# Performance work log

Measured on AMD Instinct MI355X. Metric: run time of the kernel, lower is better.

The kernel has to match this reference:

```python
import jax, jax.numpy as jnp
import numpy as np

B, T, N, D, M, H, L, FF = 8, 128, 24, 128, 9, 8, 4, 1024
F = D // H          # spatial head dim = 16
HD = D // H         # temporal head dim = 16
ND = N * D          # 3072
NM = N * M          # 216


def setup_inputs() -> dict:
    key = jax.random.key(0)
    ks = jax.random.split(key, 24)
    w = lambda k, shape, s=0.05: (jax.random.normal(k, shape, jnp.float32) * s)
    z = lambda shape: jnp.zeros(shape, jnp.float32)
    return {
        "inputs": jax.random.normal(ks[0], (B, T, NM), jnp.float32),
        "emb_W": w(ks[1], (N, M, D)), "emb_b": z((N, D)),
        "sp_Wq": w(ks[2], (L, H, N, D, F)), "sp_bq": z((L, H, N, F)),
        "sp_Wk": w(ks[3], (L, H, D, F)), "sp_bk": z((L, H, F)),
        "sp_Wv": w(ks[4], (L, H, D, F)), "sp_bv": z((L, H, F)),
        "tmp_Win": w(ks[5], (L, N, 3 * D, D)), "tmp_bin": z((L, N, 3 * D)),
        "tmp_Wout": w(ks[6], (L, N, D, D)), "tmp_bout": z((L, N, D)),
        "ff_W1": w(ks[7], (L, ND, FF)), "ff_b1": z((L, FF)),
        "ff_W2": w(ks[8], (L, FF, ND)), "ff_b2": z((L, ND)),
        "ln_g": jnp.ones((L, ND), jnp.float32), "ln_b": z((L, ND)),
        "fin_W": w(ks[9], (ND, NM)), "fin_b": z((NM,)),
    }


def _ln(x, g, b):
    m = jnp.mean(x, -1, keepdims=True)
    v = jnp.mean(jnp.square(x - m), -1, keepdims=True)
    return (x - m) * jax.lax.rsqrt(v + 1e-5) * g + b


def _pos_encoding():
    # standard sinusoidal PE; original adds it over the FIRST axis of the
    # (B, T, N*D) tensor (applied before the permute), so index by B.
    pos = jnp.arange(B, dtype=jnp.float32)[:, None]
    div = jnp.exp(jnp.arange(0, ND, 2, dtype=jnp.float32) * (-np.log(10000.0) / ND))
    pe = jnp.zeros((B, ND), jnp.float32)
    pe = pe.at[:, 0::2].set(jnp.sin(pos * div)).at[:, 1::2].set(jnp.cos(pos * div))
    return pe


def reference(inputs, emb_W, emb_b, sp_Wq, sp_bq, sp_Wk, sp_bk, sp_Wv, sp_bv,
              tmp_Win, tmp_bin, tmp_Wout, tmp_bout, ff_W1, ff_b1, ff_W2, ff_b2,
              ln_g, ln_b, fin_W, fin_b):
    # joint embedding: (B,T,N,M) @ (N,M,D) -> (B,T,N,D)
    x4 = inputs.reshape(B, T, N, M)
    emb = (jnp.einsum('btnm,nmd->btnd', x4, emb_W) + emb_b).reshape(B, T, ND)
    emb = emb + _pos_encoding()[:, None, :]
    h = emb.transpose(1, 0, 2)                     # (T, B, ND)
    # PyTorch float attn_mask is ADDED to scores: +1.0 strictly below diagonal
    mask = jnp.tril(jnp.ones((T, T), jnp.float32), -1)
    for l in range(L):
        xr = h.reshape(T, B, N, D)
        # ---- spatial attention (shared K/V, per-joint Q, per head) ----
        k = jnp.einsum('tbnd,hdf->tbhnf', xr, sp_Wk[l]) + sp_bk[l][:, None, :]
        v = jnp.einsum('tbnd,hdf->tbhnf', xr, sp_Wv[l]) + sp_bv[l][:, None, :]
        q = jnp.einsum('tbnd,hndf->tbhnf', xr, sp_Wq[l]) + sp_bq[l]
        a = jax.nn.softmax(jnp.einsum('tbhnf,tbhmf->tbhnm', q, k) / jnp.sqrt(jnp.float32(F)), -1)
        sp = jnp.einsum('tbhnm,tbhmf->tbhnf', a, v)
        sp = sp.transpose(0, 1, 3, 2, 4).reshape(T, B, ND)   # joint-major, heads concat within joint
        sp = _ln(sp + h, ln_g[l], ln_b[l])
        # ---- temporal attention (per-joint nn.MultiheadAttention) ----
        Wq_t, Wk_t, Wv_t = tmp_Win[l, :, :D], tmp_Win[l, :, D:2 * D], tmp_Win[l, :, 2 * D:]
        bq_t, bk_t, bv_t = tmp_bin[l, :, :D], tmp_bin[l, :, D:2 * D], tmp_bin[l, :, 2 * D:]
        qt = (jnp.einsum('tbnd,ned->tbne', xr, Wq_t) + bq_t).reshape(T, B, N, H, HD)
        kt = (jnp.einsum('tbnd,ned->tbne', xr, Wk_t) + bk_t).reshape(T, B, N, H, HD)
        vt = (jnp.einsum('tbnd,ned->tbne', xr, Wv_t) + bv_t).reshape(T, B, N, H, HD)
        st = jnp.einsum('tbnhe,sbnhe->bnhts', qt, kt) / jnp.sqrt(jnp.float32(HD)) + mask
        at = jax.nn.softmax(st, -1)
        ot = jnp.einsum('bnhts,sbnhe->tbnhe', at, vt).reshape(T, B, N, D)
        tp = (jnp.einsum('tbnd,nod->tbno', ot, tmp_Wout[l]) + tmp_bout[l]).reshape(T, B, ND)
        tp = _ln(tp + h, ln_g[l], ln_b[l])
        # ---- FFN (no activation in original) + residual + shared LN ----
        a2 = sp + tp
        o = (a2 @ ff_W1[l] + ff_b1[l]) @ ff_W2[l] + ff_b2[l]
        h = _ln(o + a2, ln_g[l], ln_b[l])
    out = h @ fin_W + fin_b                        # (T, B, NM)
    return out.transpose(1, 0, 2) + inputs
```

## Files before the change

### kernel.cpp

```cpp
#include <hip/hip_runtime.h>
#include <hip/hip_bf16.h>
#include <math.h>

constexpr int kB = 8, kT = 128, kN = 24, kD = 128, kM = 9, kH = 8, kL = 4, kFF = 1024;
constexpr int kF = 16;
constexpr int kHD = 16;
constexpr int kND = kN * kD;
constexpr int kNM = kN * kM;
constexpr int kP = kB * kT;

using bf16x8 = __attribute__((ext_vector_type(8))) short;
using f32x4  = __attribute__((ext_vector_type(4))) float;
typedef __hip_bfloat16 bf16;

__device__ __forceinline__ void load_lds16(const void* g, void* l) {
  __builtin_amdgcn_global_load_lds(
      (const __attribute__((address_space(1))) void*)g,
      (__attribute__((address_space(3))) void*)l, 16, 0, 0);
}

template<int BM, int BN, bool OUTBF>
__global__ __launch_bounds__(256) void mfma_gemm(
    const bf16* __restrict__ A, const bf16* __restrict__ Bm,
    const float* __restrict__ bias, void* __restrict__ Cv,
    int M, int Nc, int K, int ldB, int sAi, int sCi,
    long offAg, long offBg, long offCg, int sBg)
{
  constexpr int WM = BM / 2, WN = BN / 2;
  constexpr int MT = WM / 16, NT = WN / 16;
  constexpr int ASLOTS = BM * 8;
  constexpr int BSLOTS = BN * 8;
  constexpr int CSTR = BN + 4;
  __shared__ __align__(16) char smem[(BM + BN) * 64 * 2];
  bf16* As = (bf16*)smem;
  bf16* Bs = (bf16*)(smem + BM * 64 * 2);
  float* Cs = (float*)smem;

  int g = blockIdx.z;
  A  += offAg * g;
  Bm += offBg * g;
  long cbase = offCg * (long)g;
  int bOff = sBg * g;

  int m0 = blockIdx.y * BM, n0 = blockIdx.x * BN;
  int tid = threadIdx.x, lane = tid & 63, wave = tid >> 6;
  int wm = wave >> 1, wn = wave & 1;
  int fr = lane & 15, fq = lane >> 4;

  f32x4 acc[MT][NT] = {};

  for (int kk = 0; kk < K; kk += 64) {
#pragma unroll
    for (int s = tid; s < ASLOTS; s += 256) {
      int m = s >> 3, kq = (s & 7) ^ (m & 7);
      load_lds16(A + (size_t)(m0 + m) * sAi + (kk + kq * 8), &As[s * 8]);
    }
#pragma unroll
    for (int s = tid; s < BSLOTS; s += 256) {
      int n = s >> 3, kq = (s & 7) ^ (n & 7);
      int nr = n0 + n; if (nr > Nc - 1) nr = Nc - 1;
      load_lds16(Bm + (size_t)nr * ldB + (kk + kq * 8), &Bs[s * 8]);
    }
    __syncthreads();
#pragma unroll
    for (int ks = 0; ks < 2; ks++) {
      bf16x8 af[MT], bfr[NT];
#pragma unroll
      for (int i = 0; i < MT; i++) {
        int row = wm * WM + i * 16 + fr;
        af[i] = *(const bf16x8*)&As[row * 64 + (((ks * 4 + fq) ^ (row & 7)) * 8)];
      }
#pragma unroll
      for (int j = 0; j < NT; j++) {
        int row = wn * WN + j * 16 + fr;
        bfr[j] = *(const bf16x8*)&Bs[row * 64 + (((ks * 4 + fq) ^ (row & 7)) * 8)];
      }
#pragma unroll
      for (int i = 0; i < MT; i++)
#pragma unroll
        for (int j = 0; j < NT; j++)
          acc[i][j] = __builtin_amdgcn_mfma_f32_16x16x32_bf16(af[i], bfr[j], acc[i][j], 0, 0, 0);
    }
    __syncthreads();
  }

  constexpr int NCHUNK = BN / 16;
  int tcol = tid & (NCHUNK - 1);
  int trow = tid / NCHUNK;
  int colbase = n0 + tcol * 16;
  float vb[16];
  if (trow < 32) {
#pragma unroll
    for (int jj = 0; jj < 16; jj++)
      vb[jj] = bias ? bias[bOff + colbase + jj] : 0.f;
  }
#pragma unroll
  for (int i = 0; i < MT; i++) {
    __syncthreads();
#pragma unroll
    for (int j = 0; j < NT; j++)
#pragma unroll
      for (int r = 0; r < 4; r++)
        Cs[(wm * 16 + fq * 4 + r) * CSTR + wn * WN + j * 16 + fr] = acc[i][j][r];
    __syncthreads();
    if (trow < 32) {
      int row = m0 + (trow >> 4) * WM + i * 16 + (trow & 15);
      float vals[16];
#pragma unroll
      for (int jj = 0; jj < 4; jj++)
        *(float4*)&vals[jj * 4] = *(const float4*)&Cs[trow * CSTR + tcol * 16 + jj * 4];
#pragma unroll
      for (int jj = 0; jj < 16; jj++) vals[jj] += vb[jj];
      if (OUTBF) {
        bf16* cp = (bf16*)Cv + cbase + (size_t)row * sCi + colbase;
        union { bf16 h[8]; uint4 v; } pk;
#pragma unroll
        for (int half = 0; half < 2; half++) {
          if (colbase + half * 8 + 8 <= Nc) {
#pragma unroll
            for (int jj = 0; jj < 8; jj++) pk.h[jj] = __float2bfloat16(vals[half * 8 + jj]);
            *(uint4*)(cp + half * 8) = pk.v;
          }
        }
      } else {
        float* cp = (float*)Cv + cbase + (size_t)row * sCi + colbase;
#pragma unroll
        for (int jj = 0; jj < 4; jj++)
          if (colbase + jj * 4 + 4 <= Nc) *(float4*)(cp + jj * 4) = *(float4*)&vals[jj * 4];
      }
    }
  }
}

constexpr int NB_EMB = kP;
constexpr int NB_SPQ = kL * kH * kN;
constexpr int NB_SPK = kL * kH * kN;
constexpr int NB_SPV = kL * kH * kN;
constexpr int NB_TMP = (kL * kN * 384 * kD / 8) / 256;
constexpr int NB_CVT = (kL * 24 * 128 * 128 / 8) / 256;
constexpr int NB_SPB = (kL * 24 * 768) / 256;
constexpr int NB_W1  = (kFF / 64) * (kND / 64) * kL;
constexpr int NB_W2  = (kND / 64) * (kFF / 64) * kL;
constexpr int NB_FIN = ((kNM + 63) / 64) * (kND / 64);
constexpr int OFF_SPQ = NB_EMB;
constexpr int OFF_SPK = OFF_SPQ + NB_SPQ;
constexpr int OFF_SPV = OFF_SPK + NB_SPK;
constexpr int OFF_TMP = OFF_SPV + NB_SPV;
constexpr int OFF_CVT = OFF_TMP + NB_TMP;
constexpr int OFF_SPB = OFF_CVT + NB_CVT;
constexpr int OFF_W1  = OFF_SPB + NB_SPB;
constexpr int OFF_W2  = OFF_W1 + NB_W1;
constexpr int OFF_FIN = OFF_W2 + NB_W2;
constexpr int NB_PREP = OFF_FIN + NB_FIN;

__device__ __forceinline__ void trans_cvt_body(
    const float* __restrict__ in, bf16* __restrict__ out,
    int R, int C, int bx, int by, float (*t)[65], int tid)
{
  int c0 = bx * 64, r0 = by * 64;
  for (int s = tid; s < 1024; s += 256) {
    int rr = s >> 4, c4 = (s & 15) * 4;
    int r = r0 + rr, c = c0 + c4;
    float4 v;
    if (c + 4 <= C) v = *(const float4*)&in[(size_t)r * C + c];
    else {
      float tmp[4];
#pragma unroll
      for (int j = 0; j < 4; j++) tmp[j] = (c + j < C) ? in[(size_t)r * C + c + j] : 0.f;
      v = *(float4*)tmp;
    }
    *(float4*)&t[rr][c4] = v;
  }
  __syncthreads();
  for (int s = tid; s < 512; s += 256) {
    int cc = s >> 3, r8 = (s & 7) * 8;
    int c = c0 + cc;
    if (c < C) {
      union { bf16 h[8]; uint4 v; } pk;
#pragma unroll
      for (int j = 0; j < 8; j++) pk.h[j] = __float2bfloat16(t[r8 + j][cc]);
      *(uint4*)&out[(size_t)c * R + r0 + r8] = pk.v;
    }
  }
}

__device__ __forceinline__ void spw_transpose_body(
    const float* __restrict__ src, bf16* __restrict__ dst, float* ts, int tid)
{
  for (int s = tid; s < 512; s += 256) {
    float4 v = ((const float4*)src)[s];
    int d = s >> 2, f4 = (s & 3) * 4;
    ts[(f4 + 0) * 132 + d] = v.x;
    ts[(f4 + 1) * 132 + d] = v.y;
    ts[(f4 + 2) * 132 + d] = v.z;
    ts[(f4 + 3) * 132 + d] = v.w;
  }
  __syncthreads();
  int f = tid >> 4, d8 = (tid & 15) * 8;
  float4 a = *(const float4*)&ts[f * 132 + d8];
  float4 b = *(const float4*)&ts[f * 132 + d8 + 4];
  union { bf16 h[8]; uint4 v; } pk;
  pk.h[0] = __float2bfloat16(a.x); pk.h[1] = __float2bfloat16(a.y);
  pk.h[2] = __float2bfloat16(a.z); pk.h[3] = __float2bfloat16(a.w);
  pk.h[4] = __float2bfloat16(b.x); pk.h[5] = __float2bfloat16(b.y);
  pk.h[6] = __float2bfloat16(b.z); pk.h[7] = __float2bfloat16(b.w);
  *(uint4*)&dst[(size_t)f * 128 + d8] = pk.v;
}

__global__ __launch_bounds__(256) void prep_kernel(
    const float* __restrict__ sp_Wq, const float* __restrict__ sp_Wk,
    const float* __restrict__ sp_Wv, const float* __restrict__ tmp_Win,
    bf16* __restrict__ spW,
    const float* __restrict__ tmp_Wout, bf16* __restrict__ toWb,
    const float* __restrict__ sp_bq, const float* __restrict__ sp_bk,
    const float* __restrict__ sp_bv, const float* __restrict__ tmp_bin,
    float* __restrict__ spbc,
    const float* __restrict__ ff_W1, bf16* __restrict__ W1t,
    const float* __restrict__ ff_W2, bf16* __restrict__ W2t,
    const float* __restrict__ fin_W, bf16* __restrict__ finWt,
    const float* __restrict__ inp, const float* __restrict__ emb_W,
    const float* __restrict__ emb_b, float* __restrict__ hb,
    bf16* __restrict__ hbb)
{
  __shared__ __align__(16) char sm[64 * 65 * 4];
  int bid = blockIdx.x, tid = threadIdx.x;

  if (bid < OFF_SPQ) {
    int p = bid;
    int t = p / kB, b = p % kB;
    float* xs = (float*)sm;
    if (tid < kNM)
      xs[tid] = inp[((size_t)b * kT + t) * kNM + tid];
    __syncthreads();
    const float c1 = -logf(10000.f) / (float)kND;
    for (int c4 = tid; c4 < kND / 4; c4 += 256) {
      int c = c4 * 4;
      int n = c >> 7, d = c & 127;
      float4 acc = *(const float4*)&emb_b[n * kD + d];
#pragma unroll
      for (int m = 0; m < kM; m++) {
        float xv = xs[n * kM + m];
        float4 w = *(const float4*)&emb_W[((size_t)(n * kM + m)) * kD + d];
        acc.x += xv * w.x; acc.y += xv * w.y; acc.z += xv * w.z; acc.w += xv * w.w;
      }
      float ang0 = (float)b * expf((float)c * c1);
      float ang1 = (float)b * expf((float)(c + 2) * c1);
      acc.x += sinf(ang0); acc.y += cosf(ang0);
      acc.z += sinf(ang1); acc.w += cosf(ang1);
      *(float4*)&hb[(size_t)p * kND + c] = acc;
      union { bf16 h4[4]; uint2 v; } pk;
      pk.h4[0] = __float2bfloat16(acc.x); pk.h4[1] = __float2bfloat16(acc.y);
      pk.h4[2] = __float2bfloat16(acc.z); pk.h4[3] = __float2bfloat16(acc.w);
      *(uint2*)&hbb[(size_t)p * kND + c] = pk.v;
    }
  } else if (bid < OFF_SPK) {
    int idx = bid - OFF_SPQ;
    int l = idx / 192, rem = idx % 192;
    int hh = rem / 24, n = rem % 24;
    const float* src = sp_Wq + ((((size_t)l * kH + hh) * kN + n)) * (kD * kF);
    bf16* dst = spW + (((size_t)(l * 24 + n)) * 768 + hh * 16) * 128;
    spw_transpose_body(src, dst, (float*)sm, tid);
  } else if (bid < OFF_SPV) {
    int idx = bid - OFF_SPK;
    int l = idx / 192, rem = idx % 192;
    int hh = rem / 24, n = rem % 24;
    const float* src = sp_Wk + (((size_t)l * kH + hh)) * (kD * kF);
    bf16* dst = spW + (((size_t)(l * 24 + n)) * 768 + 128 + hh * 16) * 128;
    spw_transpose_body(src, dst, (float*)sm, tid);
  } else if (bid < OFF_TMP) {
    int idx = bid - OFF_SPV;
    int l = idx / 192, rem = idx % 192;
    int hh = rem / 24, n = rem % 24;
    const float* src = sp_Wv + (((size_t)l * kH + hh)) * (kD * kF);
    bf16* dst = spW + (((size_t)(l * 24 + n)) * 768 + 256 + hh * 16) * 128;
    spw_transpose_body(src, dst, (float*)sm, tid);
  } else if (bid < OFF_CVT) {
    long j8 = ((long)(bid - OFF_TMP) * 256 + tid) * 8;
    long ln = j8 / 49152, rem = j8 % 49152;
    const float* src = &tmp_Win[ln * 49152 + rem];
    float4 v0 = *(const float4*)src, v1 = *(const float4*)(src + 4);
    union { bf16 h[8]; uint4 v; } pk;
    pk.h[0] = __float2bfloat16(v0.x); pk.h[1] = __float2bfloat16(v0.y);
    pk.h[2] = __float2bfloat16(v0.z); pk.h[3] = __float2bfloat16(v0.w);
    pk.h[4] = __float2bfloat16(v1.x); pk.h[5] = __float2bfloat16(v1.y);
    pk.h[6] = __float2bfloat16(v1.z); pk.h[7] = __float2bfloat16(v1.w);
    *(uint4*)&spW[ln * 98304 + 49152 + rem] = pk.v;
  } else if (bid < OFF_SPB) {
    int i8 = ((bid - OFF_CVT) * 256 + tid) * 8;
    float4 v0 = *(const float4*)(tmp_Wout + i8);
    float4 v1 = *(const float4*)(tmp_Wout + i8 + 4);
    union { bf16 h[8]; uint4 v; } pk;
    pk.h[0] = __float2bfloat16(v0.x); pk.h[1] = __float2bfloat16(v0.y);
    pk.h[2] = __float2bfloat16(v0.z); pk.h[3] = __float2bfloat16(v0.w);
    pk.h[4] = __float2bfloat16(v1.x); pk.h[5] = __float2bfloat16(v1.y);
    pk.h[6] = __float2bfloat16(v1.z); pk.h[7] = __float2bfloat16(v1.w);
    *(uint4*)(toWb + i8) = pk.v;
  } else if (bid < OFF_W1) {
    int i = (bid - OFF_SPB) * 256 + tid;
    int r = i % 768;
    int n = (i / 768) % 24;
    int l = i / (768 * 24);
    int hh = (r & 127) >> 4, f = r & 15;
    float v;
    if (r < 128)      v = sp_bq[(((size_t)l * kH + hh) * kN + n) * kF + f];
    else if (r < 256) v = sp_bk[((size_t)l * kH + hh) * kF + f];
    else if (r < 384) v = sp_bv[((size_t)l * kH + hh) * kF + f];
    else              v = tmp_bin[((size_t)l * kN + n) * 384 + (r - 384)];
    spbc[i] = v;
  } else if (bid < OFF_W2) {
    int id2 = bid - OFF_W1;
    int bz = id2 / (16 * 48);
    int rem = id2 % (16 * 48);
    trans_cvt_body(ff_W1 + (size_t)bz * kND * kFF, W1t + (size_t)bz * kFF * kND,
                   kND, kFF, rem % 16, rem / 16, (float(*)[65])sm, tid);
  } else if (bid < OFF_FIN) {
    int id2 = bid - OFF_W2;
    int bz = id2 / (48 * 16);
    int rem = id2 % (48 * 16);
    trans_cvt_body(ff_W2 + (size_t)bz * kFF * kND, W2t + (size_t)bz * kND * kFF,
                   kFF, kND, rem % 48, rem / 48, (float(*)[65])sm, tid);
  } else {
    int id2 = bid - OFF_FIN;
    trans_cvt_body(fin_W, finWt, kND, kNM, id2 % 4, id2 / 4, (float(*)[65])sm, tid);
  }
}

__global__ __launch_bounds__(256) void attn_kernel(
    const bf16* __restrict__ qkv, float* __restrict__ sp_out,
    bf16* __restrict__ ot)
{
  __shared__ __align__(16) char smem[39168];
  int tid = threadIdx.x;

  if (blockIdx.x < kP) {
    int p = blockIdx.x;
    float* s = (float*)smem;
    for (int i = tid; i < 2304; i += 256) {
      int n = i / 96, c4 = (i % 96) * 4;
      ushort4 u = *(const ushort4*)((const ushort*)qkv + ((size_t)n * kP + p) * 768 + c4);
      float4 f;
      f.x = __bfloat162float(*(const bf16*)&u.x);
      f.y = __bfloat162float(*(const bf16*)&u.y);
      f.z = __bfloat162float(*(const bf16*)&u.z);
      f.w = __bfloat162float(*(const bf16*)&u.w);
      *(float4*)&s[n * 388 + c4] = f;
    }
    __syncthreads();
    if (tid < 192) {
      int hh = tid / 24, n = tid % 24;
      const float4* qr = (const float4*)(s + n * 388 + hh * 16);
      float4 q0 = qr[0], q1 = qr[1], q2 = qr[2], q3 = qr[3];
      float sc[24];
      float mx = -1e30f;
#pragma unroll
      for (int m = 0; m < 24; m++) {
        const float4* kr = (const float4*)(s + m * 388 + 128 + hh * 16);
        float4 k0 = kr[0], k1 = kr[1], k2 = kr[2], k3 = kr[3];
        float d = q0.x * k0.x + q0.y * k0.y + q0.z * k0.z + q0.w * k0.w
                + q1.x * k1.x + q1.y * k1.y + q1.z * k1.z + q1.w * k1.w
                + q2.x * k2.x + q2.y * k2.y + q2.z * k2.z + q2.w * k2.w
                + q3.x * k3.x + q3.y * k3.y + q3.z * k3.z + q3.w * k3.w;
        d *= 0.25f;
        sc[m] = d;
        mx = fmaxf(mx, d);
      }
      float sum = 0.f;
#pragma unroll
      for (int m = 0; m < 24; m++) { float e = __expf(sc[m] - mx); sc[m] = e; sum += e; }
      float inv = 1.f / sum;
      float4 o0 = {0,0,0,0}, o1 = {0,0,0,0}, o2 = {0,0,0,0}, o3 = {0,0,0,0};
#pragma unroll
      for (int m = 0; m < 24; m++) {
        const float4* vr = (const float4*)(s + m * 388 + 256 + hh * 16);
        float4 v0 = vr[0], v1 = vr[1], v2 = vr[2], v3 = vr[3];
        float w = sc[m];
        o0.x += w * v0.x; o0.y += w * v0.y; o0.z += w * v0.z; o0.w += w * v0.w;
        o1.x += w * v1.x; o1.y += w * v1.y; o1.z += w * v1.z; o1.w += w * v1.w;
        o2.x += w * v2.x; o2.y += w * v2.y; o2.z += w * v2.z; o2.w += w * v2.w;
        o3.x += w * v3.x; o3.y += w * v3.y; o3.z += w * v3.z; o3.w += w * v3.w;
      }
      float* orow = sp_out + (size_t)p * kND + n * kD + hh * 16;
      o0.x *= inv; o0.y *= inv; o0.z *= inv; o0.w *= inv;
      o1.x *= inv; o1.y *= inv; o1.z *= inv; o1.w *= inv;
      o2.x *= inv; o2.y *= inv; o2.z *= inv; o2.w *= inv;
      o3.x *= inv; o3.y *= inv; o3.z *= inv; o3.w *= inv;
      *(float4*)(orow)      = o0;
      *(float4*)(orow + 4)  = o1;
      *(float4*)(orow + 8)  = o2;
      *(float4*)(orow + 12) = o3;
    }
  } else {
    int g = blockIdx.x - kP;
    int hh = g & 7, n = (g >> 3) % 24, b = g / 192;
    ushort (*Qs)[40]  = (ushort(*)[40])(smem);
    ushort (*Ks)[40]  = (ushort(*)[40])(smem + 10240);
    ushort (*Ps)[136] = (ushort(*)[136])(smem);
    ushort (*Vt)[136] = (ushort(*)[136])(smem + 34816);

    {
      int t = tid >> 1, e8 = (tid & 1) * 8;
      const ushort* src = (const ushort*)qkv +
          ((size_t)n * kP + (size_t)t * kB + b) * 768 + 384 + hh * 16 + e8;
      uint4 q = *(const uint4*)(src);
      uint4 k = *(const uint4*)(src + 128);
      uint4 v = *(const uint4*)(src + 256);
      *(uint4*)&Qs[t][e8] = q;
      *(uint4*)&Ks[t][e8] = k;
      *(uint4*)&Qs[t][16 + e8] = make_uint4(0, 0, 0, 0);
      *(uint4*)&Ks[t][16 + e8] = make_uint4(0, 0, 0, 0);
      const ushort* vp = (const ushort*)&v;
#pragma unroll
      for (int j = 0; j < 8; j++) Vt[e8 + j][t] = vp[j];
    }
    __syncthreads();

    int lane = tid & 63, w = tid >> 6;
    int c = lane & 15, quad = lane >> 4;

    bf16x8 aq[2];
#pragma unroll
    for (int mt = 0; mt < 2; mt++)
      aq[mt] = *(const bf16x8*)&Qs[w * 32 + mt * 16 + c][quad * 8];
    f32x4 acc[2][8];
#pragma unroll
    for (int nt = 0; nt < 8; nt++) {
      bf16x8 bk = *(const bf16x8*)&Ks[nt * 16 + c][quad * 8];
#pragma unroll
      for (int mt = 0; mt < 2; mt++) {
        f32x4 z = {0.f, 0.f, 0.f, 0.f};
        acc[mt][nt] = __builtin_amdgcn_mfma_f32_16x16x32_bf16(aq[mt], bk, z, 0, 0, 0);
      }
    }
    __syncthreads();

    f32x4 invv[2];
#pragma unroll
    for (int mt = 0; mt < 2; mt++) {
      int tbase = w * 32 + mt * 16 + quad * 4;
      f32x4 rm = {-1e30f, -1e30f, -1e30f, -1e30f};
#pragma unroll
      for (int nt = 0; nt < 8; nt++) {
        int s = nt * 16 + c;
#pragma unroll
        for (int r = 0; r < 4; r++) {
          float x = acc[mt][nt][r] * 0.25f + ((s < tbase + r) ? 1.f : 0.f);
          acc[mt][nt][r] = x;
          rm[r] = fmaxf(rm[r], x);
        }
      }
#pragma unroll
      for (int off = 1; off < 16; off <<= 1)
#pragma unroll
        for (int r = 0; r < 4; r++) rm[r] = fmaxf(rm[r], __shfl_xor(rm[r], off, 64));
      f32x4 rs = {0.f, 0.f, 0.f, 0.f};
#pragma unroll
      for (int nt = 0; nt < 8; nt++)
#pragma unroll
        for (int r = 0; r < 4; r++) {
          float pp = __expf(acc[mt][nt][r] - rm[r]);
          acc[mt][nt][r] = pp;
          rs[r] += pp;
        }
#pragma unroll
      for (int off = 1; off < 16; off <<= 1)
#pragma unroll
        for (int r = 0; r < 4; r++) rs[r] += __shfl_xor(rs[r], off, 64);
#pragma unroll
      for (int r = 0; r < 4; r++) invv[mt][r] = 1.f / rs[r];
#pragma unroll
      for (int nt = 0; nt < 8; nt++)
#pragma unroll
        for (int r = 0; r < 4; r++) {
          bf16 pb = __float2bfloat16(acc[mt][nt][r]);
          Ps[tbase + r][nt * 16 + c] = *(ushort*)&pb;
        }
    }
    __syncthreads();

    f32x4 o[2] = {};
#pragma unroll
    for (int ks = 0; ks < 128; ks += 32) {
      bf16x8 bv = *(const bf16x8*)&Vt[c][ks + quad * 8];
#pragma unroll
      for (int mt = 0; mt < 2; mt++) {
        bf16x8 ap = *(const bf16x8*)&Ps[w * 32 + mt * 16 + c][ks + quad * 8];
        o[mt] = __builtin_amdgcn_mfma_f32_16x16x32_bf16(ap, bv, o[mt], 0, 0, 0);
      }
    }

#pragma unroll
    for (int mt = 0; mt < 2; mt++) {
#pragma unroll
      for (int r = 0; r < 4; r++) {
        int t = w * 32 + mt * 16 + quad * 4 + r;
        float val = o[mt][r] * invv[mt][r];
        ot[((size_t)n * kP + (size_t)t * kB + b) * 128 + hh * 16 + c] = __float2bfloat16(val);
      }
    }
  }
}

__global__ __launch_bounds__(256) void fuse_a2_kernel(
    const float* __restrict__ sp, const float* __restrict__ tp,
    const float* __restrict__ h, const float* __restrict__ g,
    const float* __restrict__ be, float* __restrict__ a2, bf16* __restrict__ a2b)
{
  int row = blockIdx.x;
  const float4* s1p = (const float4*)(sp + (size_t)row * kND);
  const float4* s2p = (const float4*)(tp + (size_t)row * kND);
  const float4* hp  = (const float4*)(h  + (size_t)row * kND);
  float4 x1[3], x2[3];
  float sum1 = 0.f, sum2 = 0.f;
#pragma unroll
  for (int i = 0; i < 3; i++) {
    int c = threadIdx.x + 256 * i;
    float4 hv = hp[c], a = s1p[c], bb = s2p[c];
    a.x += hv.x; a.y += hv.y; a.z += hv.z; a.w += hv.w;
    bb.x += hv.x; bb.y += hv.y; bb.z += hv.z; bb.w += hv.w;
    x1[i] = a; x2[i] = bb;
    sum1 += a.x + a.y + a.z + a.w;
    sum2 += bb.x + bb.y + bb.z + bb.w;
  }
  __shared__ float red1[4], red2[4];
#pragma unroll
  for (int o = 32; o > 0; o >>= 1) { sum1 += __shfl_down(sum1, o, 64); sum2 += __shfl_down(sum2, o, 64); }
  int wid = threadIdx.x >> 6;
  if ((threadIdx.x & 63) == 0) { red1[wid] = sum1; red2[wid] = sum2; }
  __syncthreads();
  float mean1 = (red1[0] + red1[1] + red1[2] + red1[3]) * (1.f / kND);
  float mean2 = (red2[0] + red2[1] + red2[2] + red2[3]) * (1.f / kND);
  __syncthreads();
  float v1 = 0.f, v2 = 0.f;
#pragma unroll
  for (int i = 0; i < 3; i++) {
    float4 a = x1[i], bb = x2[i];
    v1 += (a.x - mean1) * (a.x - mean1) + (a.y - mean1) * (a.y - mean1)
        + (a.z - mean1) * (a.z - mean1) + (a.w - mean1) * (a.w - mean1);
    v2 += (bb.x - mean2) * (bb.x - mean2) + (bb.y - mean2) * (bb.y - mean2)
        + (bb.z - mean2) * (bb.z - mean2) + (bb.w - mean2) * (bb.w - mean2);
  }
#pragma unroll
  for (int o = 32; o > 0; o >>= 1) { v1 += __shfl_down(v1, o, 64); v2 += __shfl_down(v2, o, 64); }
  if ((threadIdx.x & 63) == 0) { red1[wid] = v1; red2[wid] = v2; }
  __syncthreads();
  float r1 = rsqrtf((red1[0] + red1[1] + red1[2] + red1[3]) * (1.f / kND) + 1e-5f);
  float r2 = rsqrtf((red2[0] + red2[1] + red2[2] + red2[3]) * (1.f / kND) + 1e-5f);
  const float4* g4 = (const float4*)g;
  const float4* b4 = (const float4*)be;
#pragma unroll
  for (int i = 0; i < 3; i++) {
    int c = threadIdx.x + 256 * i;
    float4 gc = g4[c], bc = b4[c];
    float4 a = x1[i], bb = x2[i], o;
    o.x = (a.x - mean1) * r1 * gc.x + bc.x + (bb.x - mean2) * r2 * gc.x + bc.x;
    o.y = (a.y - mean1) * r1 * gc.y + bc.y + (bb.y - mean2) * r2 * gc.y + bc.y;
    o.z = (a.z - mean1) * r1 * gc.z + bc.z + (bb.z - mean2) * r2 * gc.z + bc.z;
    o.w = (a.w - mean1) * r1 * gc.w + bc.w + (bb.w - mean2) * r2 * gc.w + bc.w;
    *(float4*)(a2 + (size_t)row * kND + c * 4) = o;
    union { bf16 h4[4]; uint2 v; } pk;
    pk.h4[0] = __float2bfloat16(o.x); pk.h4[1] = __float2bfloat16(o.y);
    pk.h4[2] = __float2bfloat16(o.z); pk.h4[3] = __float2bfloat16(o.w);
    *(uint2*)(a2b + (size_t)row * kND + c * 4) = pk.v;
  }
}

__global__ __launch_bounds__(256) void add_ln_dual_kernel(
    const float* __restrict__ a, const float* __restrict__ b,
    const float* __restrict__ g, const float* __restrict__ be,
    float* __restrict__ out, bf16* __restrict__ outb)
{
  int row = blockIdx.x;
  const float4* ar = (const float4*)(a + (size_t)row * kND);
  const float4* br = (const float4*)(b + (size_t)row * kND);
  float4 v[3];
  float s = 0.f;
#pragma unroll
  for (int i = 0; i < 3; i++) {
    int c = threadIdx.x + 256 * i;
    float4 x = ar[c], y = br[c];
    x.x += y.x; x.y += y.y; x.z += y.z; x.w += y.w;
    v[i] = x;
    s += x.x + x.y + x.z + x.w;
  }
  __shared__ float red[4];
#pragma unroll
  for (int o = 32; o > 0; o >>= 1) s += __shfl_down(s, o, 64);
  int wid = threadIdx.x >> 6;
  if ((threadIdx.x & 63) == 0) red[wid] = s;
  __syncthreads();
  float mean = (red[0] + red[1] + red[2] + red[3]) * (1.f / kND);
  __syncthreads();
  float vs = 0.f;
#pragma unroll
  for (int i = 0; i < 3; i++) {
    float4 x = v[i];
    vs += (x.x - mean) * (x.x - mean) + (x.y - mean) * (x.y - mean)
        + (x.z - mean) * (x.z - mean) + (x.w - mean) * (x.w - mean);
  }
#pragma unroll
  for (int o = 32; o > 0; o >>= 1) vs += __shfl_down(vs, o, 64);
  if ((threadIdx.x & 63) == 0) red[wid] = vs;
  __syncthreads();
  float rstd = rsqrtf((red[0] + red[1] + red[2] + red[3]) * (1.f / kND) + 1e-5f);
  const float4* g4 = (const float4*)g;
  const float4* b4 = (const float4*)be;
#pragma unroll
  for (int i = 0; i < 3; i++) {
    int c = threadIdx.x + 256 * i;
    float4 gc = g4[c], bc = b4[c], x = v[i], o;
    o.x = (x.x - mean) * rstd * gc.x + bc.x;
    o.y = (x.y - mean) * rstd * gc.y + bc.y;
    o.z = (x.z - mean) * rstd * gc.z + bc.z;
    o.w = (x.w - mean) * rstd * gc.w + bc.w;
    *(float4*)(out + (size_t)row * kND + c * 4) = o;
    union { bf16 h4[4]; uint2 v2; } pk;
    pk.h4[0] = __float2bfloat16(o.x); pk.h4[1] = __float2bfloat16(o.y);
    pk.h4[2] = __float2bfloat16(o.z); pk.h4[3] = __float2bfloat16(o.w);
    *(uint2*)(outb + (size_t)row * kND + c * 4) = pk.v2;
  }
}

__global__ __launch_bounds__(256) void ff1_reduce_kernel(
    const float* __restrict__ part, const float* __restrict__ bias,
    bf16* __restrict__ out)
{
  int i4 = (blockIdx.x * 256 + threadIdx.x) * 4;
  const size_t S = (size_t)kP * kFF;
  float4 p0 = *(const float4*)(part + i4);
  float4 p1 = *(const float4*)(part + S + i4);
  float4 p2 = *(const float4*)(part + 2 * S + i4);
  int col = i4 & (kFF - 1);
  float4 bb = *(const float4*)(bias + col);
  union { bf16 h4[4]; uint2 v; } pk;
  pk.h4[0] = __float2bfloat16(p0.x + p1.x + p2.x + bb.x);
  pk.h4[1] = __float2bfloat16(p0.y + p1.y + p2.y + bb.y);
  pk.h4[2] = __float2bfloat16(p0.z + p1.z + p2.z + bb.z);
  pk.h4[3] = __float2bfloat16(p0.w + p1.w + p2.w + bb.w);
  *(uint2*)(out + i4) = pk.v;
}

__global__ __launch_bounds__(256) void final_reduce_add_kernel(
    const float* __restrict__ part, const float* __restrict__ fin_b,
    const float* __restrict__ inp, float* __restrict__ out)
{
  int i = blockIdx.x * 256 + threadIdx.x;
  if (i >= kB * kT * kNM) return;
  int c = i % kNM;
  int rem = i / kNM;
  int t = rem % kT, b = rem / kT;
  size_t pi = (size_t)(t * kB + b) * kNM + c;
  const size_t S = (size_t)kP * kNM;
  float v = fin_b[c] + inp[i];
#pragma unroll
  for (int z = 0; z < 8; z++) v += part[z * S + pi];
  out[i] = v;
}

extern "C" void kernel_launch(void* const* d_in, const int* in_sizes, int n_in,
                              void* d_out, int out_size, void* d_ws, size_t ws_size,
                              hipStream_t stream)
{
  const float* inputs   = (const float*)d_in[0];
  const float* emb_W    = (const float*)d_in[1];
  const float* emb_b    = (const float*)d_in[2];
  const float* sp_Wq    = (const float*)d_in[3];
  const float* sp_bq    = (const float*)d_in[4];
  const float* sp_Wk    = (const float*)d_in[5];
  const float* sp_bk    = (const float*)d_in[6];
  const float* sp_Wv    = (const float*)d_in[7];
  const float* sp_bv    = (const float*)d_in[8];
  const float* tmp_Win  = (const float*)d_in[9];
  const float* tmp_bin  = (const float*)d_in[10];
  const float* tmp_Wout = (const float*)d_in[11];
  const float* tmp_bout = (const float*)d_in[12];
  const float* ff_W1    = (const float*)d_in[13];
  const float* ff_b1    = (const float*)d_in[14];
  const float* ff_W2    = (const float*)d_in[15];
  const float* ff_b2    = (const float*)d_in[16];
  const float* ln_g     = (const float*)d_in[17];
  const float* ln_b     = (const float*)d_in[18];
  const float* fin_W    = (const float*)d_in[19];
  const float* fin_b    = (const float*)d_in[20];
  float* out = (float*)d_out;

  char* wp = (char*)d_ws;
  size_t off = 0;
  auto alloc = [&](size_t bytes) { void* p = wp + off; off += (bytes + 255) & ~(size_t)255; return p; };
  bf16* spW   = (bf16*)alloc((size_t)kL * 24 * 768 * 128 * 2);
  bf16* toWb  = (bf16*)alloc((size_t)kL * 24 * 128 * 128 * 2);
  bf16* W1t   = (bf16*)alloc((size_t)kL * kFF * kND * 2);
  bf16* W2t   = (bf16*)alloc((size_t)kL * kND * kFF * 2);
  bf16* finWt = (bf16*)alloc((size_t)kNM * kND * 2);
  float* spbc = (float*)alloc((size_t)kL * 24 * 768 * 4);
  float* hb   = (float*)alloc((size_t)kP * kND * 4);
  bf16*  hbb  = (bf16*) alloc((size_t)kP * kND * 2);
  bf16*  qkvb = (bf16*) alloc((size_t)24 * kP * 768 * 2);
  float* sp   = (float*)alloc((size_t)kP * kND * 4);
  float* tp   = (float*)alloc((size_t)kP * kND * 4);
  float* a2   = (float*)alloc((size_t)kP * kND * 4);
  bf16*  a2b  = (bf16*) alloc((size_t)kP * kND * 2);
  bf16*  f1b  = (bf16*) alloc((size_t)kP * kFF * 2);
  bf16*  otb  = (bf16*) alloc((size_t)24 * kP * 128 * 2);
  float* ffpart  = sp;
  float* finpart = tp;

  prep_kernel<<<NB_PREP, 256, 0, stream>>>(
      sp_Wq, sp_Wk, sp_Wv, tmp_Win, spW,
      tmp_Wout, toWb,
      sp_bq, sp_bk, sp_bv, tmp_bin, spbc,
      ff_W1, W1t, ff_W2, W2t, fin_W, finWt,
      inputs, emb_W, emb_b, hb, hbb);

  for (int l = 0; l < kL; l++) {
    const float* lg = ln_g + (size_t)l * kND;
    const float* lb = ln_b + (size_t)l * kND;

    mfma_gemm<128, 128, true><<<dim3(6, 8, 24), 256, 0, stream>>>(
        hbb, spW + (size_t)l * 24 * 768 * 128, spbc + (size_t)l * 24 * 768, qkvb,
        kP, 768, 128, 128, kND, 768,
        128, 768 * 128, (long)kP * 768, 768);

    attn_kernel<<<kP + kB * 24 * 8, 256, 0, stream>>>(qkvb, sp, otb);

    mfma_gemm<64, 64, false><<<dim3(2, 16, 24), 256, 0, stream>>>(
        otb, toWb + (size_t)l * 24 * 128 * 128, tmp_bout + (size_t)l * 24 * 128, tp,
        kP, 128, 128, 128, 128, kND,
        (long)kP * 128, 128 * 128, 128, 128);

    fuse_a2_kernel<<<kP, 256, 0, stream>>>(sp, tp, hb, lg, lb, a2, a2b);

    mfma_gemm<64, 64, false><<<dim3(kFF / 64, kP / 64, 3), 256, 0, stream>>>(
        a2b, W1t + (size_t)l * kFF * kND, nullptr, ffpart,
        kP, kFF, kND / 3, kND, kND, kFF,
        kND / 3, kND / 3, (long)kP * kFF, 0);
    ff1_reduce_kernel<<<(kP * kFF / 4) / 256, 256, 0, stream>>>(
        ffpart, ff_b1 + (size_t)l * kFF, f1b);

    mfma_gemm<64, 64, false><<<dim3(kND / 64, kP / 64, 1), 256, 0, stream>>>(
        f1b, W2t + (size_t)l * kND * kFF, ff_b2 + (size_t)l * kND, tp,
        kP, kND, kFF, kFF, kFF, kND, 0, 0, 0, 0);

    add_ln_dual_kernel<<<kP, 256, 0, stream>>>(tp, a2, lg, lb, hb, hbb);
  }

  mfma_gemm<64, 64, false><<<dim3((kNM + 63) / 64, kP / 64, 8), 256, 0, stream>>>(
      hbb, finWt, nullptr, finpart,
      kP, kNM, kND / 8, kND, kND, kNM,
      kND / 8, kND / 8, (long)kP * kNM, 0);
  final_reduce_add_kernel<<<(kB * kT * kNM + 255) / 256, 256, 0, stream>>>(
      finpart, fin_b, inputs, out);
}
```

Before: 723.5 us.

## Fuse split-K reductions into GEMM via atomic last-block tile counters

```diff
diff --git a/kernel.cpp b/kernel.cpp
--- a/kernel.cpp
+++ b/kernel.cpp
@@ -19,12 +19,14 @@
       (__attribute__((address_space(3))) void*)l, 16, 0, 0);
 }
 
-template<int BM, int BN, bool OUTBF>
+template<int BM, int BN, bool OUTBF, int NZ = 0>
 __global__ __launch_bounds__(256) void mfma_gemm(
     const bf16* __restrict__ A, const bf16* __restrict__ Bm,
     const float* __restrict__ bias, void* __restrict__ Cv,
     int M, int Nc, int K, int ldB, int sAi, int sCi,
-    long offAg, long offBg, long offCg, int sBg)
+    long offAg, long offBg, long offCg, int sBg,
+    int* cnt = nullptr, const float* rbias = nullptr,
+    const float* rinp = nullptr, void* rout = nullptr)
 {
   constexpr int WM = BM / 2, WN = BN / 2;
   constexpr int MT = WM / 16, NT = WN / 16;
@@ -128,6 +130,60 @@
         for (int jj = 0; jj < 4; jj++)
           if (colbase + jj * 4 + 4 <= Nc) *(float4*)(cp + jj * 4) = *(float4*)&vals[jj * 4];
       }
+    }
+  }
+
+  if constexpr (NZ > 0) {
+    __shared__ int lastv;
+    __threadfence();
+    __syncthreads();
+    int tileId = blockIdx.y * gridDim.x + blockIdx.x;
+    if (tid == 0) lastv = atomicAdd(&cnt[tileId], 1);
+    __syncthreads();
+    if (lastv == NZ - 1) {
+      __threadfence();
+      const size_t S = (size_t)offCg;
+      int row = m0 + (tid >> 2);
+      int c0 = n0 + (tid & 3) * 16;
+      if constexpr (NZ == 3) {
+        bf16* outp = (bf16*)rout + (size_t)row * sCi;
+        const float* base = (const float*)Cv + (size_t)row * sCi;
+#pragma unroll
+        for (int q = 0; q < 4; q++) {
+          int c = c0 + q * 4;
+          float4 p0 = *(const float4*)(base + c);
+          float4 p1 = *(const float4*)(base + S + c);
+          float4 p2 = *(const float4*)(base + 2 * S + c);
+          float4 bb = *(const float4*)(rbias + c);
+          union { bf16 h4[4]; uint2 v; } pk;
+          pk.h4[0] = __float2bfloat16(p0.x + p1.x + p2.x + bb.x);
+          pk.h4[1] = __float2bfloat16(p0.y + p1.y + p2.y + bb.y);
+          pk.h4[2] = __float2bfloat16(p0.z + p1.z + p2.z + bb.z);
+          pk.h4[3] = __float2bfloat16(p0.w + p1.w + p2.w + bb.w);
+          *(uint2*)(outp + c) = pk.v;
+        }
+      } else {
+        int bb_ = row % kB, tt_ = row / kB;
+        float* outp = (float*)rout + ((size_t)bb_ * kT + tt_) * kNM;
+        const float* inpr = rinp + ((size_t)bb_ * kT + tt_) * kNM;
+        const float* base = (const float*)Cv + (size_t)row * sCi;
+#pragma unroll
+        for (int q = 0; q < 4; q++) {
+          int c = c0 + q * 4;
+          if (c + 4 <= Nc) {
+            float4 v = *(const float4*)(rbias + c);
+            float4 iv = *(const float4*)(inpr + c);
+            v.x += iv.x; v.y += iv.y; v.z += iv.z; v.w += iv.w;
+#pragma unroll
+            for (int z = 0; z < 8; z++) {
+              float4 pz = *(const float4*)(base + (size_t)z * S + c);
+              v.x += pz.x; v.y += pz.y; v.z += pz.z; v.w += pz.w;
+            }
+            *(float4*)(outp + c) = v;
+          }
+        }
+      }
+      if (tid == 0) cnt[tileId] = 0;
     }
   }
 }
@@ -151,7 +207,9 @@
 constexpr int OFF_W1  = OFF_SPB + NB_SPB;
 constexpr int OFF_W2  = OFF_W1 + NB_W1;
 constexpr int OFF_FIN = OFF_W2 + NB_W2;
-constexpr int NB_PREP = OFF_FIN + NB_FIN;
+constexpr int OFF_ZC  = OFF_FIN + NB_FIN;
+constexpr int NB_PREP = OFF_ZC + 1;
+constexpr int kNCNT = 256 + 64;
 
 __device__ __forceinline__ void trans_cvt_body(
     const float* __restrict__ in, bf16* __restrict__ out,
@@ -220,7 +278,7 @@
     const float* __restrict__ fin_W, bf16* __restrict__ finWt,
     const float* __restrict__ inp, const float* __restrict__ emb_W,
     const float* __restrict__ emb_b, float* __restrict__ hb,
-    bf16* __restrict__ hbb)
+    bf16* __restrict__ hbb, int* __restrict__ cnts)
 {
   __shared__ __align__(16) char sm[64 * 65 * 4];
   int bid = blockIdx.x, tid = threadIdx.x;
@@ -319,9 +377,11 @@
     int rem = id2 % (48 * 16);
     trans_cvt_body(ff_W2 + (size_t)bz * kFF * kND, W2t + (size_t)bz * kND * kFF,
                    kFF, kND, rem % 48, rem / 48, (float(*)[65])sm, tid);
-  } else {
+  } else if (bid < OFF_ZC) {
     int id2 = bid - OFF_FIN;
     trans_cvt_body(fin_W, finWt, kND, kNM, id2 % 4, id2 / 4, (float(*)[65])sm, tid);
+  } else {
+    for (int i = tid; i < kNCNT; i += 256) cnts[i] = 0;
   }
 }
 
@@ -618,42 +678,6 @@
     pk.h4[2] = __float2bfloat16(o.z); pk.h4[3] = __float2bfloat16(o.w);
     *(uint2*)(outb + (size_t)row * kND + c * 4) = pk.v2;
   }
-}
-
-__global__ __launch_bounds__(256) void ff1_reduce_kernel(
-    const float* __restrict__ part, const float* __restrict__ bias,
-    bf16* __restrict__ out)
-{
-  int i4 = (blockIdx.x * 256 + threadIdx.x) * 4;
-  const size_t S = (size_t)kP * kFF;
-  float4 p0 = *(const float4*)(part + i4);
-  float4 p1 = *(const float4*)(part + S + i4);
-  float4 p2 = *(const float4*)(part + 2 * S + i4);
-  int col = i4 & (kFF - 1);
-  float4 bb = *(const float4*)(bias + col);
-  union { bf16 h4[4]; uint2 v; } pk;
-  pk.h4[0] = __float2bfloat16(p0.x + p1.x + p2.x + bb.x);
-  pk.h4[1] = __float2bfloat16(p0.y + p1.y + p2.y + bb.y);
-  pk.h4[2] = __float2bfloat16(p0.z + p1.z + p2.z + bb.z);
-  pk.h4[3] = __float2bfloat16(p0.w + p1.w + p2.w + bb.w);
-  *(uint2*)(out + i4) = pk.v;
-}
-
-__global__ __launch_bounds__(256) void final_reduce_add_kernel(
-    const float* __restrict__ part, const float* __restrict__ fin_b,
-    const float* __restrict__ inp, float* __restrict__ out)
-{
-  int i = blockIdx.x * 256 + threadIdx.x;
-  if (i >= kB * kT * kNM) return;
-  int c = i % kNM;
-  int rem = i / kNM;
-  int t = rem % kT, b = rem / kT;
-  size_t pi = (size_t)(t * kB + b) * kNM + c;
-  const size_t S = (size_t)kP * kNM;
-  float v = fin_b[c] + inp[i];
-#pragma unroll
-  for (int z = 0; z < 8; z++) v += part[z * S + pi];
-  out[i] = v;
 }
 
 extern "C" void kernel_launch(void* const* d_in, const int* in_sizes, int n_in,
@@ -701,6 +725,7 @@
   bf16*  a2b  = (bf16*) alloc((size_t)kP * kND * 2);
   bf16*  f1b  = (bf16*) alloc((size_t)kP * kFF * 2);
   bf16*  otb  = (bf16*) alloc((size_t)24 * kP * 128 * 2);
+  int*   cnts = (int*)  alloc((size_t)kNCNT * 4);
   float* ffpart  = sp;
   float* finpart = tp;
 
@@ -709,7 +734,7 @@
       tmp_Wout, toWb,
       sp_bq, sp_bk, sp_bv, tmp_bin, spbc,
       ff_W1, W1t, ff_W2, W2t, fin_W, finWt,
-      inputs, emb_W, emb_b, hb, hbb);
+      inputs, emb_W, emb_b, hb, hbb, cnts);
 
   for (int l = 0; l < kL; l++) {
     const float* lg = ln_g + (size_t)l * kND;
@@ -729,12 +754,11 @@
 
     fuse_a2_kernel<<<kP, 256, 0, stream>>>(sp, tp, hb, lg, lb, a2, a2b);
 
-    mfma_gemm<64, 64, false><<<dim3(kFF / 64, kP / 64, 3), 256, 0, stream>>>(
+    mfma_gemm<64, 64, false, 3><<<dim3(kFF / 64, kP / 64, 3), 256, 0, stream>>>(
         a2b, W1t + (size_t)l * kFF * kND, nullptr, ffpart,
         kP, kFF, kND / 3, kND, kND, kFF,
-        kND / 3, kND / 3, (long)kP * kFF, 0);
-    ff1_reduce_kernel<<<(kP * kFF / 4) / 256, 256, 0, stream>>>(
-        ffpart, ff_b1 + (size_t)l * kFF, f1b);
+        kND / 3, kND / 3, (long)kP * kFF, 0,
+        cnts, ff_b1 + (size_t)l * kFF, nullptr, f1b);
 
     mfma_gemm<64, 64, false><<<dim3(kND / 64, kP / 64, 1), 256, 0, stream>>>(
         f1b, W2t + (size_t)l * kND * kFF, ff_b2 + (size_t)l * kND, tp,
@@ -743,10 +767,9 @@
     add_ln_dual_kernel<<<kP, 256, 0, stream>>>(tp, a2, lg, lb, hb, hbb);
   }
 
-  mfma_gemm<64, 64, false><<<dim3((kNM + 63) / 64, kP / 64, 8), 256, 0, stream>>>(
+  mfma_gemm<64, 64, false, 8><<<dim3((kNM + 63) / 64, kP / 64, 8), 256, 0, stream>>>(
       hbb, finWt, nullptr, finpart,
       kP, kNM, kND / 8, kND, kND, kNM,
-      kND / 8, kND / 8, (long)kP * kNM, 0);
-  final_reduce_add_kernel<<<(kB * kT * kNM + 255) / 256, 256, 0, stream>>>(
-      finpart, fin_b, inputs, out);
-}
+      kND / 8, kND / 8, (long)kP * kNM, 0,
+      cnts + 256, fin_b, inputs, out);
+}
```

New measurement: 1.365 ms. +88.7%, slower.
